# Optimization experiments

Measured on AMD Instinct MI355X. Metric: run time of the kernel, lower is better.

The kernel has to match this reference:

```python
import jax, jax.numpy as jnp
import numpy as np

BLANK = 0
NEG = jnp.float32(-1e30)  # finite stand-in for -inf (keeps logaddexp grads NaN-free)


def _ctc_loss(preds, targets, blank=BLANK):
    """CTC loss with fused log_softmax, zero_infinity, reduction='mean'.

    preds:   (N, T, C) raw logits
    targets: (N, L) int labels, 0 = padding/blank; target_lengths = count_nonzero
    """
    N, T, C = preds.shape
    L = targets.shape[1]
    S = 2 * L + 1  # extended label length (blanks interleaved)

    lp = jax.nn.log_softmax(preds, axis=-1)  # (N, T, C)

    # extended label sequence: blank, y1, blank, y2, ..., yL, blank
    ext = jnp.full((N, S), blank, dtype=targets.dtype).at[:, 1::2].set(targets)

    # gather log-probs of extended labels: (N, T, S) -> scan over T as (T, N, S)
    lp_ext = jax.vmap(lambda l, e: l[:, e])(lp, ext).transpose(1, 0, 2)

    # skip transition s-2 -> s allowed iff ext[s] != blank and ext[s] != ext[s-2]
    prev2 = jnp.pad(ext, ((0, 0), (2, 0)), constant_values=blank)[:, :S]
    skip_ok = (ext != blank) & (ext != prev2)  # (N, S)

    # alpha init at t=0
    alpha0 = jnp.full((N, S), NEG, dtype=lp.dtype)
    alpha0 = alpha0.at[:, 0].set(lp_ext[0, :, 0]).at[:, 1].set(lp_ext[0, :, 1])

    neg_col = jnp.full((N, 1), NEG, dtype=lp.dtype)

    def step(alpha, lp_t):
        a1 = jnp.concatenate([neg_col, alpha[:, :-1]], axis=1)
        a2 = jnp.concatenate([neg_col, neg_col, alpha[:, :-2]], axis=1)
        a2 = jnp.where(skip_ok, a2, NEG)
        alpha = jnp.logaddexp(jnp.logaddexp(alpha, a1), a2) + lp_t
        return alpha, None

    alpha, _ = jax.lax.scan(step, alpha0, lp_ext[1:])  # (N, S) at t = T-1

    tl = jnp.sum(targets != 0, axis=1)  # target lengths (pred lengths are all T)
    rows = jnp.arange(N)
    final = jnp.logaddexp(alpha[rows, 2 * tl], alpha[rows, 2 * tl - 1])

    # zero_infinity=True: zero out non-finite (vanished) losses
    loss = jnp.where(final < -1e29, 0.0, -final)
    # reduction='mean': divide each by its target length, then batch-mean
    return jnp.mean(loss / jnp.maximum(tl, 1).astype(loss.dtype))


def setup_inputs() -> dict:
    key = jax.random.key(0)
    k1, k2 = jax.random.split(key)
    preds = jax.random.normal(k1, (128, 1024, 256), dtype=jnp.float32)
    # labels in [1, C): nonzero so count_nonzero gives full target lengths
    targets = jax.random.randint(k2, (128, 128), 1, 256, dtype=jnp.int32)
    return {"preds": preds, "targets": targets}


def reference(preds, targets):
    return _ctc_loss(preds, targets)
```

## Files before the change

### kernel.cpp

```cpp
#include <hip/hip_runtime.h>

#define L2E 1.4426950408889634f
#define LN2D 0.6931471805599453

__device__ __forceinline__ void async_copy16(const float* g, float* l) {
    __builtin_amdgcn_global_load_lds(
        (const __attribute__((address_space(1))) void*)g,
        (__attribute__((address_space(3))) void*)l, 16, 0, 0);
}
__device__ __forceinline__ void wait_vm14() { __builtin_amdgcn_s_waitcnt(0x0F7E); }

__device__ __forceinline__ double dpp_sr1_f64(double x) {
    const int lo = __builtin_amdgcn_update_dpp(0, __double2loint(x), 0x138, 0xF, 0xF, true);
    const int hi = __builtin_amdgcn_update_dpp(0, __double2hiint(x), 0x138, 0xF, 0xF, true);
    return __hiloint2double(hi, lo);
}

__device__ __forceinline__ int wave_imax(int v) {
    int t;
#define DM(ctrl) t = __builtin_amdgcn_update_dpp(v, v, (ctrl), 0xF, 0xF, false); v = (v > t) ? v : t
    DM(0x111); DM(0x112); DM(0x114); DM(0x118);
    DM(0x142); DM(0x143);
#undef DM
    return __builtin_amdgcn_readlane(v, 63);
}

__global__ __launch_bounds__(256) void gather_kernel(const float* __restrict__ preds,
                                                     const int* __restrict__ targets,
                                                     float* __restrict__ gath,
                                                     float* __restrict__ blank) {
    constexpr int T = 1024, C = 256, L = 128;
    const int n = blockIdx.x >> 6;
    const int c = ((blockIdx.x & 63) << 2) + (threadIdx.x >> 6);
    const int lane = threadIdx.x & 63;
    const int w = threadIdx.x >> 6;

    const float* __restrict__ P = preds + ((size_t)n * T + (size_t)c * 4) * C;
    const int* __restrict__ tg = targets + (size_t)n * L;
    const int tgA = tg[2 * lane + 0];
    const int tgB = tg[2 * lane + 1];

    __shared__ float sRow[4][4][C];
    float m_k[4], r_k[4];
#pragma unroll
    for (int k = 0; k < 4; ++k) {
        const float4 v = reinterpret_cast<const float4*>(P + (size_t)k * C)[lane];
        reinterpret_cast<float4*>(&sRow[w][k][0])[lane] = v;
        float m = fmaxf(fmaxf(v.x, v.y), fmaxf(v.z, v.w));
#pragma unroll
        for (int off = 32; off; off >>= 1) m = fmaxf(m, __shfl_xor(m, off, 64));
        float s = exp2f((v.x - m) * L2E) + exp2f((v.y - m) * L2E) +
                  exp2f((v.z - m) * L2E) + exp2f((v.w - m) * L2E);
#pragma unroll
        for (int off = 32; off; off >>= 1) s += __shfl_xor(s, off, 64);
        m_k[k] = m; r_k[k] = 1.0f / s;
    }
    float4 gA, gB;
    gA.x = exp2f((sRow[w][0][tgA] - m_k[0]) * L2E) * r_k[0];
    gA.y = exp2f((sRow[w][1][tgA] - m_k[1]) * L2E) * r_k[1];
    gA.z = exp2f((sRow[w][2][tgA] - m_k[2]) * L2E) * r_k[2];
    gA.w = exp2f((sRow[w][3][tgA] - m_k[3]) * L2E) * r_k[3];
    gB.x = exp2f((sRow[w][0][tgB] - m_k[0]) * L2E) * r_k[0];
    gB.y = exp2f((sRow[w][1][tgB] - m_k[1]) * L2E) * r_k[1];
    gB.z = exp2f((sRow[w][2][tgB] - m_k[2]) * L2E) * r_k[2];
    gB.w = exp2f((sRow[w][3][tgB] - m_k[3]) * L2E) * r_k[3];

    float* gp = gath + ((size_t)n * 256 + c) * 512;
    *reinterpret_cast<float4*>(gp + 4 * lane) = gA;
    *reinterpret_cast<float4*>(gp + 256 + 4 * lane) = gB;
    if (lane == 0) {
        float4 b;
        b.x = exp2f((sRow[w][0][0] - m_k[0]) * L2E) * r_k[0];
        b.y = exp2f((sRow[w][1][0] - m_k[1]) * L2E) * r_k[1];
        b.z = exp2f((sRow[w][2][0] - m_k[2]) * L2E) * r_k[2];
        b.w = exp2f((sRow[w][3][0] - m_k[3]) * L2E) * r_k[3];
        *reinterpret_cast<float4*>(blank + (size_t)n * T + (size_t)c * 4) = b;
    }
}

__global__ __launch_bounds__(64) void ctc_alpha_kernel(const float* __restrict__ gath,
                                                       const float* __restrict__ blank,
                                                       const int* __restrict__ targets,
                                                       float* __restrict__ loss_out) {
    constexpr int T = 1024, L = 128, DIST = 8;
    __shared__ float sG[16 * 512];
    __shared__ float sBlank[T];
    __shared__ double sFin[257];

    const int n = blockIdx.x;
    const int lane = threadIdx.x;
    const int* __restrict__ tg = targets + (size_t)n * L;

    const int tA = tg[2 * lane + 0];
    const int tB = tg[2 * lane + 1];
    int tPrev = __shfl_up(tB, 1, 64);
    if (lane == 0) tPrev = 0;
    const bool skipA = (tA != 0) && (tA != tPrev);
    const bool skipB = (tB != 0) && (tB != tA);

    int cnt = (tA != 0) + (tB != 0);
#pragma unroll
    for (int off = 32; off; off >>= 1) cnt += __shfl_xor(cnt, off, 64);
    const int tl = cnt;

    const float* __restrict__ gn = gath + (size_t)n * 131072;
    const float* __restrict__ bn = blank + (size_t)n * T;

#pragma unroll
    for (int i = 0; i < 4; ++i) async_copy16(bn + i * 256 + lane * 4, &sBlank[i * 256]);
#pragma unroll
    for (int c = 0; c < DIST; ++c) {
        async_copy16(gn + c * 512 + lane * 4, &sG[c * 512]);
        async_copy16(gn + c * 512 + 256 + lane * 4, &sG[c * 512 + 256]);
    }

    double A0, A1, A2, A3, A4;
    double sc = 1.0;
    int e_apply = 0, K = 0;

#define LOADCHUNK(CC, AF, BF, BB) do {                                          \
        wait_vm14();                                                            \
        const int slot_ = (CC) & 15;                                            \
        AF = *reinterpret_cast<const float4*>(&sG[slot_ * 512 + 4 * lane]);     \
        BF = *reinterpret_cast<const float4*>(&sG[slot_ * 512 + 256 + 4 * lane]); \
        BB = *reinterpret_cast<const float4*>(&sBlank[4 * (CC)]);               \
        const int cp_ = (CC) + DIST, sp_ = cp_ & 15;                            \
        async_copy16(gn + cp_ * 512 + lane * 4, &sG[sp_ * 512]);                \
        async_copy16(gn + cp_ * 512 + 256 + lane * 4, &sG[sp_ * 512 + 256]);    \
    } while (0)

#define STEP(PB, PA, PB2) do {                                                  \
        const double p3 = dpp_sr1_f64(A3);                                      \
        const double u0 = A0 + p3;                                              \
        const double u1 = A1 + A0 + (skipA ? p3 : 0.0);                         \
        const double u2 = A2 + A1;                                              \
        const double u3 = A3 + A2 + (skipB ? A1 : 0.0);                         \
        const double u4 = A4 + A3;                                              \
        A0 = u0 * (PB); A1 = u1 * (PA); A2 = u2 * (PB);                         \
        A3 = u3 * (PB2); A4 = u4 * (PB);                                        \
    } while (0)

#define DOCHUNK(CC) do {                                                        \
        float4 Af_, Bf_, bb_;                                                   \
        LOADCHUNK(CC, Af_, Bf_, bb_);                                           \
        STEP((double)bb_.x, (double)Af_.x, (double)Bf_.x);                      \
        STEP((double)bb_.y, (double)Af_.y, (double)Bf_.y);                      \
        STEP((double)bb_.z, (double)Af_.z, (double)Bf_.z);                      \
        STEP((double)bb_.w, (double)Af_.w, (double)Bf_.w);                      \
    } while (0)

#define RESCALE() do {                                                          \
        A0 *= sc; A1 *= sc; A2 *= sc; A3 *= sc; A4 *= sc; K += e_apply;         \
        const double m_ = fmax(fmax(fmax(A0, A1), fmax(A2, A3)), A4);           \
        int e_ = ((__double2hiint(m_) >> 20) & 0x7FF) - 1023;                   \
        e_ = wave_imax(e_);                                                     \
        e_ = e_ < -960 ? -960 : (e_ > 960 ? 960 : e_);                          \
        e_apply = e_;                                                           \
        sc = __hiloint2double((1023 - e_) << 20, 0);                            \
    } while (0)

    {
        float4 Af_, Bf_, bb_;
        LOADCHUNK(0, Af_, Bf_, bb_);
        A0 = lane ? 0.0 : (double)bb_.x;
        A1 = lane ? 0.0 : (double)Af_.x;
        A2 = 0.0; A3 = 0.0; A4 = 0.0;
        STEP((double)bb_.y, (double)Af_.y, (double)Bf_.y);
        STEP((double)bb_.z, (double)Af_.z, (double)Bf_.z);
        STEP((double)bb_.w, (double)Af_.w, (double)Bf_.w);
    }
    for (int c = 1; c < 255; c += 2) {
        DOCHUNK(c);
        RESCALE();
        DOCHUNK(c + 1);
    }
    DOCHUNK(255);
    RESCALE();
#undef RESCALE
#undef DOCHUNK
#undef STEP
#undef LOADCHUNK

    sFin[4 * lane + 0] = A0; sFin[4 * lane + 1] = A1;
    sFin[4 * lane + 2] = A2; sFin[4 * lane + 3] = A3;
    if (lane == 63) sFin[256] = A4;
    __syncthreads();
    if (lane == 0) {
        int i1 = 2 * tl;
        int i0 = 2 * tl - 1;
        if (i0 < 0) i0 += 257;
        if (i1 > 256) i1 = 256;
        const double fin = sFin[i1] + sFin[i0];
        const double loss = (fin > 0.0) ? -(log2(fin) + (double)K) * LN2D : 0.0;
        loss_out[n] = (float)(loss / (double)(tl > 0 ? tl : 1));
    }
}

__global__ __launch_bounds__(64) void reduce_kernel(const float* __restrict__ loss,
                                                    float* __restrict__ out, int N) {
    float s = 0.0f;
    for (int i = threadIdx.x; i < N; i += 64) s += loss[i];
#pragma unroll
    for (int off = 32; off; off >>= 1) s += __shfl_xor(s, off, 64);
    if (threadIdx.x == 0) out[0] = s / (float)N;
}

extern "C" void kernel_launch(void* const* d_in, const int* in_sizes, int n_in,
                              void* d_out, int out_size, void* d_ws, size_t ws_size,
                              hipStream_t stream) {
    const float* preds = (const float*)d_in[0];
    const int* targets = (const int*)d_in[1];
    const int N = in_sizes[1] / 128;
    const int T = 1024;

    float* gath = (float*)d_ws;
    float* blank = gath + (size_t)N * 131072;
    float* loss = blank + (size_t)N * T;
    float* out = (float*)d_out;

    gather_kernel<<<N * 64, 256, 0, stream>>>(preds, targets, gath, blank);
    ctc_alpha_kernel<<<N, 64, 0, stream>>>(gath, blank, targets, loss);
    reduce_kernel<<<1, 64, 0, stream>>>(loss, out, N);
}
```

Baseline: 282.2 us.

## Split CTC recursion into interleaved forward-alpha and backward-beta halves

The single forward alpha recursion over all 1024 timesteps becomes a forward alpha pass over the first half and a backward beta pass over the second half. The two independent chains are interleaved step by step, and the loss is formed from a wave-reduced dot product of alpha and beta at the midpoint. This halves the serial dependency chain and exposes instruction-level parallelism. The cost is double register state and separate rescaling for each chain. Async prefetch now streams chunks from both ends of the gathered buffer.

```diff
diff --git a/kernel.cpp b/kernel.cpp
--- a/kernel.cpp
+++ b/kernel.cpp
@@ -8,14 +8,19 @@
         (const __attribute__((address_space(1))) void*)g,
         (__attribute__((address_space(3))) void*)l, 16, 0, 0);
 }
-__device__ __forceinline__ void wait_vm14() { __builtin_amdgcn_s_waitcnt(0x0F7E); }
+__device__ __forceinline__ void wait_vm28() { __builtin_amdgcn_s_waitcnt(0x4F7C); }
+__device__ __forceinline__ void wait_vm0()  { __builtin_amdgcn_s_waitcnt(0x0F70); }
 
 __device__ __forceinline__ double dpp_sr1_f64(double x) {
     const int lo = __builtin_amdgcn_update_dpp(0, __double2loint(x), 0x138, 0xF, 0xF, true);
     const int hi = __builtin_amdgcn_update_dpp(0, __double2hiint(x), 0x138, 0xF, 0xF, true);
     return __hiloint2double(hi, lo);
 }
-
+__device__ __forceinline__ double dpp_sl1_f64(double x) {
+    const int lo = __builtin_amdgcn_update_dpp(0, __double2loint(x), 0x130, 0xF, 0xF, true);
+    const int hi = __builtin_amdgcn_update_dpp(0, __double2hiint(x), 0x130, 0xF, 0xF, true);
+    return __hiloint2double(hi, lo);
+}
 __device__ __forceinline__ int wave_imax(int v) {
     int t;
 #define DM(ctrl) t = __builtin_amdgcn_update_dpp(v, v, (ctrl), 0xF, 0xF, false); v = (v > t) ? v : t
@@ -82,10 +87,9 @@
                                                        const float* __restrict__ blank,
                                                        const int* __restrict__ targets,
                                                        float* __restrict__ loss_out) {
-    constexpr int T = 1024, L = 128, DIST = 8;
+    constexpr int T = 1024, L = 128;
     __shared__ float sG[16 * 512];
     __shared__ float sBlank[T];
-    __shared__ double sFin[257];
 
     const int n = blockIdx.x;
     const int lane = threadIdx.x;
@@ -95,41 +99,50 @@
     const int tB = tg[2 * lane + 1];
     int tPrev = __shfl_up(tB, 1, 64);
     if (lane == 0) tPrev = 0;
-    const bool skipA = (tA != 0) && (tA != tPrev);
+    const int skipAi = (tA != 0 && tA != tPrev) ? 1 : 0;
+    const bool skipA = skipAi != 0;
     const bool skipB = (tB != 0) && (tB != tA);
+    const double mBd = skipB ? 1.0 : 0.0;
+    const double mA1d = (double)__shfl_down(skipAi, 1, 64);
 
     int cnt = (tA != 0) + (tB != 0);
 #pragma unroll
     for (int off = 32; off; off >>= 1) cnt += __shfl_xor(cnt, off, 64);
     const int tl = cnt;
+    int i1 = 2 * tl;       if (i1 > 256) i1 = 256;
+    int i0 = 2 * tl - 1;   if (i0 < 0) i0 += 257;
 
     const float* __restrict__ gn = gath + (size_t)n * 131072;
     const float* __restrict__ bn = blank + (size_t)n * T;
 
+    wait_vm0();
+
 #pragma unroll
     for (int i = 0; i < 4; ++i) async_copy16(bn + i * 256 + lane * 4, &sBlank[i * 256]);
 #pragma unroll
-    for (int c = 0; c < DIST; ++c) {
-        async_copy16(gn + c * 512 + lane * 4, &sG[c * 512]);
-        async_copy16(gn + c * 512 + 256 + lane * 4, &sG[c * 512 + 256]);
+    for (int i = 0; i < 8; ++i) {
+        async_copy16(gn + i * 512 + lane * 4,       &sG[i * 512]);
+        async_copy16(gn + i * 512 + 256 + lane * 4, &sG[i * 512 + 256]);
+        const int q = 255 - i;
+        async_copy16(gn + q * 512 + lane * 4,       &sG[(8 + i) * 512]);
+        async_copy16(gn + q * 512 + 256 + lane * 4, &sG[(8 + i) * 512 + 256]);
     }
 
     double A0, A1, A2, A3, A4;
-    double sc = 1.0;
-    int e_apply = 0, K = 0;
-
-#define LOADCHUNK(CC, AF, BF, BB) do {                                          \
-        wait_vm14();                                                            \
-        const int slot_ = (CC) & 15;                                            \
-        AF = *reinterpret_cast<const float4*>(&sG[slot_ * 512 + 4 * lane]);     \
-        BF = *reinterpret_cast<const float4*>(&sG[slot_ * 512 + 256 + 4 * lane]); \
-        BB = *reinterpret_cast<const float4*>(&sBlank[4 * (CC)]);               \
-        const int cp_ = (CC) + DIST, sp_ = cp_ & 15;                            \
-        async_copy16(gn + cp_ * 512 + lane * 4, &sG[sp_ * 512]);                \
-        async_copy16(gn + cp_ * 512 + 256 + lane * 4, &sG[sp_ * 512 + 256]);    \
-    } while (0)
-
-#define STEP(PB, PA, PB2) do {                                                  \
+    double B0, B1, B2, B3, B4;
+    double scA = 1.0, scB = 1.0;
+    int eA = 0, eB = 0, KA = 0, KB = 0;
+
+    {
+        const int s0 = 4 * lane;
+        B0 = (s0 == i1 || s0 == i0) ? 1.0 : 0.0;
+        B1 = (s0 + 1 == i1 || s0 + 1 == i0) ? 1.0 : 0.0;
+        B2 = (s0 + 2 == i1 || s0 + 2 == i0) ? 1.0 : 0.0;
+        B3 = (s0 + 3 == i1 || s0 + 3 == i0) ? 1.0 : 0.0;
+        B4 = (lane == 63 && (i1 == 256 || i0 == 256)) ? 1.0 : 0.0;
+    }
+
+#define ASTEP(PB, PA, PB2) do {                                                 \
         const double p3 = dpp_sr1_f64(A3);                                      \
         const double u0 = A0 + p3;                                              \
         const double u1 = A1 + A0 + (skipA ? p3 : 0.0);                         \
@@ -140,58 +153,88 @@
         A3 = u3 * (PB2); A4 = u4 * (PB);                                        \
     } while (0)
 
-#define DOCHUNK(CC) do {                                                        \
-        float4 Af_, Bf_, bb_;                                                   \
-        LOADCHUNK(CC, Af_, Bf_, bb_);                                           \
-        STEP((double)bb_.x, (double)Af_.x, (double)Bf_.x);                      \
-        STEP((double)bb_.y, (double)Af_.y, (double)Bf_.y);                      \
-        STEP((double)bb_.z, (double)Af_.z, (double)Bf_.z);                      \
-        STEP((double)bb_.w, (double)Af_.w, (double)Bf_.w);                      \
-    } while (0)
-
-#define RESCALE() do {                                                          \
-        A0 *= sc; A1 *= sc; A2 *= sc; A3 *= sc; A4 *= sc; K += e_apply;         \
-        const double m_ = fmax(fmax(fmax(A0, A1), fmax(A2, A3)), A4);           \
-        int e_ = ((__double2hiint(m_) >> 20) & 0x7FF) - 1023;                   \
-        e_ = wave_imax(e_);                                                     \
-        e_ = e_ < -960 ? -960 : (e_ > 960 ? 960 : e_);                          \
-        e_apply = e_;                                                           \
-        sc = __hiloint2double((1023 - e_) << 20, 0);                            \
-    } while (0)
-
-    {
-        float4 Af_, Bf_, bb_;
-        LOADCHUNK(0, Af_, Bf_, bb_);
-        A0 = lane ? 0.0 : (double)bb_.x;
-        A1 = lane ? 0.0 : (double)Af_.x;
-        A2 = 0.0; A3 = 0.0; A4 = 0.0;
-        STEP((double)bb_.y, (double)Af_.y, (double)Bf_.y);
-        STEP((double)bb_.z, (double)Af_.z, (double)Bf_.z);
-        STEP((double)bb_.w, (double)Af_.w, (double)Bf_.w);
-    }
-    for (int c = 1; c < 255; c += 2) {
-        DOCHUNK(c);
-        RESCALE();
-        DOCHUNK(c + 1);
-    }
-    DOCHUNK(255);
-    RESCALE();
-#undef RESCALE
-#undef DOCHUNK
-#undef STEP
-#undef LOADCHUNK
-
-    sFin[4 * lane + 0] = A0; sFin[4 * lane + 1] = A1;
-    sFin[4 * lane + 2] = A2; sFin[4 * lane + 3] = A3;
-    if (lane == 63) sFin[256] = A4;
-    __syncthreads();
+#define BSTEP(PBF, PAF, PBF2) do {                                              \
+        const double pb_ = (PBF);                                               \
+        const double g0 = pb_ * B0;                                             \
+        const double g1 = (PAF) * B1;                                           \
+        const double g2 = pb_ * B2;                                             \
+        const double g3 = (PBF2) * B3;                                          \
+        const double g4 = pb_ * B4;                                             \
+        double G4 = dpp_sl1_f64(g0);                                            \
+        G4 = (lane == 63) ? g4 : G4;                                            \
+        const double G5 = dpp_sl1_f64(g1);                                      \
+        B0 = g0 + g1;                                                           \
+        B1 = fma(mBd, g3, g1 + g2);                                             \
+        B2 = g2 + g3;                                                           \
+        B3 = fma(mA1d, G5, g3 + G4);                                            \
+        B4 = g4;                                                                \
+    } while (0)
+
+#define PAIRBODY(P_, FIRST_)  do {                                              \
+        const int sl_ = (P_) & 7;                                               \
+        wait_vm28();                                                            \
+        const float4 aA = *reinterpret_cast<const float4*>(&sG[sl_ * 512 + 4 * lane]);        \
+        const float4 aB = *reinterpret_cast<const float4*>(&sG[sl_ * 512 + 256 + 4 * lane]);  \
+        const float4 ab = *reinterpret_cast<const float4*>(&sBlank[4 * (P_)]);                \
+        const float4 bA = *reinterpret_cast<const float4*>(&sG[(8 + sl_) * 512 + 4 * lane]);       \
+        const float4 bB = *reinterpret_cast<const float4*>(&sG[(8 + sl_) * 512 + 256 + 4 * lane]); \
+        const float4 bb = *reinterpret_cast<const float4*>(&sBlank[4 * (255 - (P_))]);        \
+        { const int cp = (P_) + 8, q = 247 - (P_);                              \
+          async_copy16(gn + cp * 512 + lane * 4,       &sG[sl_ * 512]);         \
+          async_copy16(gn + cp * 512 + 256 + lane * 4, &sG[sl_ * 512 + 256]);   \
+          async_copy16(gn + q * 512 + lane * 4,        &sG[(8 + sl_) * 512]);   \
+          async_copy16(gn + q * 512 + 256 + lane * 4,  &sG[(8 + sl_) * 512 + 256]); } \
+        if (FIRST_) {                                                           \
+            A0 = lane ? 0.0 : (double)ab.x;                                     \
+            A1 = lane ? 0.0 : (double)aA.x;                                     \
+            A2 = 0.0; A3 = 0.0; A4 = 0.0;                                       \
+        } else {                                                                \
+            ASTEP((double)ab.x, (double)aA.x, (double)aB.x);                    \
+        }                                                                       \
+        BSTEP((double)bb.w, (double)bA.w, (double)bB.w);                        \
+        ASTEP((double)ab.y, (double)aA.y, (double)aB.y);                        \
+        BSTEP((double)bb.z, (double)bA.z, (double)bB.z);                        \
+        ASTEP((double)ab.z, (double)aA.z, (double)aB.z);                        \
+        BSTEP((double)bb.y, (double)bA.y, (double)bB.y);                        \
+        ASTEP((double)ab.w, (double)aA.w, (double)aB.w);                        \
+        BSTEP((double)bb.x, (double)bA.x, (double)bB.x);                        \
+    } while (0)
+
+#define RESCALES() do {                                                         \
+        A0 *= scA; A1 *= scA; A2 *= scA; A3 *= scA; A4 *= scA; KA += eA;        \
+        B0 *= scB; B1 *= scB; B2 *= scB; B3 *= scB; B4 *= scB; KB += eB;        \
+        const double ma = fmax(fmax(fmax(A0, A1), fmax(A2, A3)), A4);           \
+        const double mb = fmax(fmax(fmax(B0, B1), fmax(B2, B3)), B4);           \
+        int ea_ = ((__double2hiint(ma) >> 20) & 0x7FF) - 1023;                  \
+        int eb_ = ((__double2hiint(mb) >> 20) & 0x7FF) - 1023;                  \
+        ea_ = wave_imax(ea_); eb_ = wave_imax(eb_);                             \
+        ea_ = ea_ < -960 ? -960 : (ea_ > 960 ? 960 : ea_);                      \
+        eb_ = eb_ < -960 ? -960 : (eb_ > 960 ? 960 : eb_);                      \
+        eA = ea_; scA = __hiloint2double((1023 - ea_) << 20, 0);                \
+        eB = eb_; scB = __hiloint2double((1023 - eb_) << 20, 0);                \
+    } while (0)
+
+    PAIRBODY(0, true);
+    for (int p = 1; p < 127; p += 2) {
+        PAIRBODY(p, false);
+        RESCALES();
+        PAIRBODY(p + 1, false);
+    }
+    PAIRBODY(127, false);
+    RESCALES();
+    A0 *= scA; A1 *= scA; A2 *= scA; A3 *= scA; A4 *= scA; KA += eA;
+    B0 *= scB; B1 *= scB; B2 *= scB; B3 *= scB; B4 *= scB; KB += eB;
+#undef RESCALES
+#undef PAIRBODY
+#undef BSTEP
+#undef ASTEP
+
+    double S = A0 * B0 + A1 * B1 + A2 * B2 + A3 * B3;
+    S += (lane == 63) ? A4 * B4 : 0.0;
+#pragma unroll
+    for (int off = 32; off; off >>= 1) S += __shfl_xor(S, off, 64);
     if (lane == 0) {
-        int i1 = 2 * tl;
-        int i0 = 2 * tl - 1;
-        if (i0 < 0) i0 += 257;
-        if (i1 > 256) i1 = 256;
-        const double fin = sFin[i1] + sFin[i0];
-        const double loss = (fin > 0.0) ? -(log2(fin) + (double)K) * LN2D : 0.0;
+        const double loss = (S > 0.0) ? -(log2(S) + (double)(KA + KB)) * LN2D : 0.0;
         loss_out[n] = (float)(loss / (double)(tl > 0 ? tl : 1));
     }
 }
```

Result: faster. 265.5 us (-5.9%).

## Fuse softmax-gather into CTC recursion with split forward/backward halves and producer waves

Applied to the files above, without the earlier changes.

Replaces the separate gather kernel and alpha kernel with one fused kernel. Three producer waves compute the softmax and gathered probabilities for 4-timestep chunks into shared-memory slots, while one consumer wave runs the recursion. Each utterance is split across two blocks: one runs the forward alpha pass over the first half of time and the other runs a backward beta pass from the final states over the second half. A combine kernel then takes the dot product of the two halves to get each loss. This removes the large gathered intermediate from global memory and halves the serial dependency chain per block. In exchange it adds per-round block barriers and a more intricate final combine.

```diff
diff --git a/kernel.cpp b/kernel.cpp
--- a/kernel.cpp
+++ b/kernel.cpp
@@ -8,14 +8,19 @@
         (const __attribute__((address_space(1))) void*)g,
         (__attribute__((address_space(3))) void*)l, 16, 0, 0);
 }
-__device__ __forceinline__ void wait_vm14() { __builtin_amdgcn_s_waitcnt(0x0F7E); }
+__device__ __forceinline__ void wait_vm0() { __builtin_amdgcn_s_waitcnt(0x0F70); }
+__device__ __forceinline__ void wait_vm4() { __builtin_amdgcn_s_waitcnt(0x0F74); }
 
 __device__ __forceinline__ double dpp_sr1_f64(double x) {
     const int lo = __builtin_amdgcn_update_dpp(0, __double2loint(x), 0x138, 0xF, 0xF, true);
     const int hi = __builtin_amdgcn_update_dpp(0, __double2hiint(x), 0x138, 0xF, 0xF, true);
     return __hiloint2double(hi, lo);
 }
-
+__device__ __forceinline__ double dpp_sl1_f64(double x) {
+    const int lo = __builtin_amdgcn_update_dpp(0, __double2loint(x), 0x130, 0xF, 0xF, true);
+    const int hi = __builtin_amdgcn_update_dpp(0, __double2hiint(x), 0x130, 0xF, 0xF, true);
+    return __hiloint2double(hi, lo);
+}
 __device__ __forceinline__ int wave_imax(int v) {
     int t;
 #define DM(ctrl) t = __builtin_amdgcn_update_dpp(v, v, (ctrl), 0xF, 0xF, false); v = (v > t) ? v : t
@@ -25,27 +30,13 @@
     return __builtin_amdgcn_readlane(v, 63);
 }
 
-__global__ __launch_bounds__(256) void gather_kernel(const float* __restrict__ preds,
-                                                     const int* __restrict__ targets,
-                                                     float* __restrict__ gath,
-                                                     float* __restrict__ blank) {
-    constexpr int T = 1024, C = 256, L = 128;
-    const int n = blockIdx.x >> 6;
-    const int c = ((blockIdx.x & 63) << 2) + (threadIdx.x >> 6);
-    const int lane = threadIdx.x & 63;
-    const int w = threadIdx.x >> 6;
-
-    const float* __restrict__ P = preds + ((size_t)n * T + (size_t)c * 4) * C;
-    const int* __restrict__ tg = targets + (size_t)n * L;
-    const int tgA = tg[2 * lane + 0];
-    const int tgB = tg[2 * lane + 1];
-
-    __shared__ float sRow[4][4][C];
-    float m_k[4], r_k[4];
+__device__ __forceinline__ void produce_chunk(const float* __restrict__ row,
+                                              float* __restrict__ slot,
+                                              int lane, int tA, int tB) {
+    float mk[4], rk[4];
 #pragma unroll
     for (int k = 0; k < 4; ++k) {
-        const float4 v = reinterpret_cast<const float4*>(P + (size_t)k * C)[lane];
-        reinterpret_cast<float4*>(&sRow[w][k][0])[lane] = v;
+        const float4 v = *reinterpret_cast<const float4*>(&row[k * 256 + 4 * lane]);
         float m = fmaxf(fmaxf(v.x, v.y), fmaxf(v.z, v.w));
 #pragma unroll
         for (int off = 32; off; off >>= 1) m = fmaxf(m, __shfl_xor(m, off, 64));
@@ -53,156 +44,231 @@
                   exp2f((v.z - m) * L2E) + exp2f((v.w - m) * L2E);
 #pragma unroll
         for (int off = 32; off; off >>= 1) s += __shfl_xor(s, off, 64);
-        m_k[k] = m; r_k[k] = 1.0f / s;
+        mk[k] = m; rk[k] = 1.0f / s;
     }
     float4 gA, gB;
-    gA.x = exp2f((sRow[w][0][tgA] - m_k[0]) * L2E) * r_k[0];
-    gA.y = exp2f((sRow[w][1][tgA] - m_k[1]) * L2E) * r_k[1];
-    gA.z = exp2f((sRow[w][2][tgA] - m_k[2]) * L2E) * r_k[2];
-    gA.w = exp2f((sRow[w][3][tgA] - m_k[3]) * L2E) * r_k[3];
-    gB.x = exp2f((sRow[w][0][tgB] - m_k[0]) * L2E) * r_k[0];
-    gB.y = exp2f((sRow[w][1][tgB] - m_k[1]) * L2E) * r_k[1];
-    gB.z = exp2f((sRow[w][2][tgB] - m_k[2]) * L2E) * r_k[2];
-    gB.w = exp2f((sRow[w][3][tgB] - m_k[3]) * L2E) * r_k[3];
-
-    float* gp = gath + ((size_t)n * 256 + c) * 512;
-    *reinterpret_cast<float4*>(gp + 4 * lane) = gA;
-    *reinterpret_cast<float4*>(gp + 256 + 4 * lane) = gB;
+    gA.x = exp2f((row[0 * 256 + tA] - mk[0]) * L2E) * rk[0];
+    gA.y = exp2f((row[1 * 256 + tA] - mk[1]) * L2E) * rk[1];
+    gA.z = exp2f((row[2 * 256 + tA] - mk[2]) * L2E) * rk[2];
+    gA.w = exp2f((row[3 * 256 + tA] - mk[3]) * L2E) * rk[3];
+    gB.x = exp2f((row[0 * 256 + tB] - mk[0]) * L2E) * rk[0];
+    gB.y = exp2f((row[1 * 256 + tB] - mk[1]) * L2E) * rk[1];
+    gB.z = exp2f((row[2 * 256 + tB] - mk[2]) * L2E) * rk[2];
+    gB.w = exp2f((row[3 * 256 + tB] - mk[3]) * L2E) * rk[3];
+    *reinterpret_cast<float4*>(&slot[4 * lane]) = gA;
+    *reinterpret_cast<float4*>(&slot[256 + 4 * lane]) = gB;
     if (lane == 0) {
-        float4 b;
-        b.x = exp2f((sRow[w][0][0] - m_k[0]) * L2E) * r_k[0];
-        b.y = exp2f((sRow[w][1][0] - m_k[1]) * L2E) * r_k[1];
-        b.z = exp2f((sRow[w][2][0] - m_k[2]) * L2E) * r_k[2];
-        b.w = exp2f((sRow[w][3][0] - m_k[3]) * L2E) * r_k[3];
-        *reinterpret_cast<float4*>(blank + (size_t)n * T + (size_t)c * 4) = b;
-    }
-}
-
-__global__ __launch_bounds__(64) void ctc_alpha_kernel(const float* __restrict__ gath,
-                                                       const float* __restrict__ blank,
-                                                       const int* __restrict__ targets,
-                                                       float* __restrict__ loss_out) {
-    constexpr int T = 1024, L = 128, DIST = 8;
-    __shared__ float sG[16 * 512];
-    __shared__ float sBlank[T];
-    __shared__ double sFin[257];
-
-    const int n = blockIdx.x;
-    const int lane = threadIdx.x;
+        float4 bb;
+        bb.x = exp2f((row[0 * 256] - mk[0]) * L2E) * rk[0];
+        bb.y = exp2f((row[1 * 256] - mk[1]) * L2E) * rk[1];
+        bb.z = exp2f((row[2 * 256] - mk[2]) * L2E) * rk[2];
+        bb.w = exp2f((row[3 * 256] - mk[3]) * L2E) * rk[3];
+        *reinterpret_cast<float4*>(&slot[512]) = bb;
+    }
+}
+
+__global__ __launch_bounds__(256) void ctc_fused_kernel(
+        const float* __restrict__ preds, const int* __restrict__ targets,
+        double* __restrict__ Aws, double* __restrict__ Bws, int* __restrict__ meta) {
+    constexpr int T = 1024, L = 128, NCH = 128;
+    __shared__ float sSlot[6][520];
+    __shared__ float sRowBuf[3][2][4 * 256];
+
+    const int n = blockIdx.x >> 1;
+    const int h = blockIdx.x & 1;
+    const int wv = threadIdx.x >> 6;
+    const int lane = threadIdx.x & 63;
+
     const int* __restrict__ tg = targets + (size_t)n * L;
-
     const int tA = tg[2 * lane + 0];
     const int tB = tg[2 * lane + 1];
+    const float* __restrict__ Pn = preds + (size_t)n * T * 256;
+
     int tPrev = __shfl_up(tB, 1, 64);
     if (lane == 0) tPrev = 0;
-    const bool skipA = (tA != 0) && (tA != tPrev);
+    const int skipAi = (tA != 0 && tA != tPrev) ? 1 : 0;
+    const bool skipA = skipAi != 0;
     const bool skipB = (tB != 0) && (tB != tA);
-
+    const double mBd = skipB ? 1.0 : 0.0;
+    const double mA1d = (double)__shfl_down(skipAi, 1, 64);
     int cnt = (tA != 0) + (tB != 0);
 #pragma unroll
     for (int off = 32; off; off >>= 1) cnt += __shfl_xor(cnt, off, 64);
     const int tl = cnt;
-
-    const float* __restrict__ gn = gath + (size_t)n * 131072;
-    const float* __restrict__ bn = blank + (size_t)n * T;
-
-#pragma unroll
-    for (int i = 0; i < 4; ++i) async_copy16(bn + i * 256 + lane * 4, &sBlank[i * 256]);
-#pragma unroll
-    for (int c = 0; c < DIST; ++c) {
-        async_copy16(gn + c * 512 + lane * 4, &sG[c * 512]);
-        async_copy16(gn + c * 512 + 256 + lane * 4, &sG[c * 512 + 256]);
-    }
-
-    double A0, A1, A2, A3, A4;
+    int i1 = 2 * tl;     if (i1 > 256) i1 = 256;
+    int i0 = 2 * tl - 1; if (i0 < 0) i0 += 257;
+
+    double X0 = 0.0, X1 = 0.0, X2 = 0.0, X3 = 0.0, X4 = 0.0;
+    if (h == 1) {
+        const int s0 = 4 * lane;
+        X0 = (s0 == i1 || s0 == i0) ? 1.0 : 0.0;
+        X1 = (s0 + 1 == i1 || s0 + 1 == i0) ? 1.0 : 0.0;
+        X2 = (s0 + 2 == i1 || s0 + 2 == i0) ? 1.0 : 0.0;
+        X3 = (s0 + 3 == i1 || s0 + 3 == i0) ? 1.0 : 0.0;
+        X4 = (lane == 63 && (i1 == 256 || i0 == 256)) ? 1.0 : 0.0;
+    }
     double sc = 1.0;
     int e_apply = 0, K = 0;
 
-#define LOADCHUNK(CC, AF, BF, BB) do {                                          \
-        wait_vm14();                                                            \
-        const int slot_ = (CC) & 15;                                            \
-        AF = *reinterpret_cast<const float4*>(&sG[slot_ * 512 + 4 * lane]);     \
-        BF = *reinterpret_cast<const float4*>(&sG[slot_ * 512 + 256 + 4 * lane]); \
-        BB = *reinterpret_cast<const float4*>(&sBlank[4 * (CC)]);               \
-        const int cp_ = (CC) + DIST, sp_ = cp_ & 15;                            \
-        async_copy16(gn + cp_ * 512 + lane * 4, &sG[sp_ * 512]);                \
-        async_copy16(gn + cp_ * 512 + 256 + lane * 4, &sG[sp_ * 512 + 256]);    \
+#define ASTEP(PBf, PAf, PB2f) do {                                              \
+        const double PB = (double)(PBf), PA = (double)(PAf), PB2 = (double)(PB2f); \
+        const double p3 = dpp_sr1_f64(X3);                                      \
+        const double u0 = X0 + p3;                                              \
+        const double u1 = X1 + X0 + (skipA ? p3 : 0.0);                         \
+        const double u2 = X2 + X1;                                              \
+        const double u3 = X3 + X2 + (skipB ? X1 : 0.0);                         \
+        const double u4 = X4 + X3;                                              \
+        X0 = u0 * PB; X1 = u1 * PA; X2 = u2 * PB; X3 = u3 * PB2; X4 = u4 * PB;  \
     } while (0)
 
-#define STEP(PB, PA, PB2) do {                                                  \
-        const double p3 = dpp_sr1_f64(A3);                                      \
-        const double u0 = A0 + p3;                                              \
-        const double u1 = A1 + A0 + (skipA ? p3 : 0.0);                         \
-        const double u2 = A2 + A1;                                              \
-        const double u3 = A3 + A2 + (skipB ? A1 : 0.0);                         \
-        const double u4 = A4 + A3;                                              \
-        A0 = u0 * (PB); A1 = u1 * (PA); A2 = u2 * (PB);                         \
-        A3 = u3 * (PB2); A4 = u4 * (PB);                                        \
+#define BSTEP(PBf, PAf, PB2f) do {                                              \
+        const double pb_ = (double)(PBf);                                       \
+        const double g0 = pb_ * X0;                                             \
+        const double g1 = (double)(PAf) * X1;                                   \
+        const double g2 = pb_ * X2;                                             \
+        const double g3 = (double)(PB2f) * X3;                                  \
+        const double g4 = pb_ * X4;                                             \
+        double G4 = dpp_sl1_f64(g0);                                            \
+        G4 = (lane == 63) ? g4 : G4;                                            \
+        const double G5 = dpp_sl1_f64(g1);                                      \
+        X0 = g0 + g1;                                                           \
+        X1 = fma(mBd, g3, g1 + g2);                                             \
+        X2 = g2 + g3;                                                           \
+        X3 = fma(mA1d, G5, g3 + G4);                                            \
+        X4 = g4;                                                                \
     } while (0)
 
-#define DOCHUNK(CC) do {                                                        \
-        float4 Af_, Bf_, bb_;                                                   \
-        LOADCHUNK(CC, Af_, Bf_, bb_);                                           \
-        STEP((double)bb_.x, (double)Af_.x, (double)Bf_.x);                      \
-        STEP((double)bb_.y, (double)Af_.y, (double)Bf_.y);                      \
-        STEP((double)bb_.z, (double)Af_.z, (double)Bf_.z);                      \
-        STEP((double)bb_.w, (double)Af_.w, (double)Bf_.w);                      \
-    } while (0)
-
 #define RESCALE() do {                                                          \
-        A0 *= sc; A1 *= sc; A2 *= sc; A3 *= sc; A4 *= sc; K += e_apply;         \
-        const double m_ = fmax(fmax(fmax(A0, A1), fmax(A2, A3)), A4);           \
+        X0 *= sc; X1 *= sc; X2 *= sc; X3 *= sc; X4 *= sc; K += e_apply;         \
+        const double m_ = fmax(fmax(fmax(X0, X1), fmax(X2, X3)), X4);           \
         int e_ = ((__double2hiint(m_) >> 20) & 0x7FF) - 1023;                   \
         e_ = wave_imax(e_);                                                     \
         e_ = e_ < -960 ? -960 : (e_ > 960 ? 960 : e_);                          \
-        e_apply = e_;                                                           \
-        sc = __hiloint2double((1023 - e_) << 20, 0);                            \
+        e_apply = e_; sc = __hiloint2double((1023 - e_) << 20, 0);              \
     } while (0)
 
-    {
-        float4 Af_, Bf_, bb_;
-        LOADCHUNK(0, Af_, Bf_, bb_);
-        A0 = lane ? 0.0 : (double)bb_.x;
-        A1 = lane ? 0.0 : (double)Af_.x;
-        A2 = 0.0; A3 = 0.0; A4 = 0.0;
-        STEP((double)bb_.y, (double)Af_.y, (double)Bf_.y);
-        STEP((double)bb_.z, (double)Af_.z, (double)Bf_.z);
-        STEP((double)bb_.w, (double)Af_.w, (double)Bf_.w);
-    }
-    for (int c = 1; c < 255; c += 2) {
-        DOCHUNK(c);
-        RESCALE();
-        DOCHUNK(c + 1);
-    }
-    DOCHUNK(255);
-    RESCALE();
+    wait_vm0();
+
+    if (wv > 0) {
+        const int pw = wv - 1;
+        const int gc0 = h ? 255 - pw : pw;
+#pragma unroll
+        for (int k = 0; k < 4; ++k)
+            async_copy16(Pn + (size_t)(4 * gc0 + k) * 256 + 4 * lane, &sRowBuf[pw][0][k * 256]);
+        wait_vm0();
+        produce_chunk(&sRowBuf[pw][0][0], &sSlot[pw][0], lane, tA, tB);
+        const int gc1 = h ? 255 - (pw + 3) : (pw + 3);
+#pragma unroll
+        for (int k = 0; k < 4; ++k)
+            async_copy16(Pn + (size_t)(4 * gc1 + k) * 256 + 4 * lane, &sRowBuf[pw][1][k * 256]);
+    }
+    __syncthreads();
+
+    for (int r = 0; r < 43; ++r) {
+        if (wv > 0) {
+            const int pw = wv - 1;
+            const int cp = 3 * (r + 1) + pw;
+            const int cn = cp + 3;
+            if (cn < NCH) {
+                const int gcn = h ? 255 - cn : cn;
+                float* dst = &sRowBuf[pw][r & 1][0];
+#pragma unroll
+                for (int k = 0; k < 4; ++k)
+                    async_copy16(Pn + (size_t)(4 * gcn + k) * 256 + 4 * lane, dst + k * 256);
+            }
+            if (cp < NCH) {
+                if (cn < NCH) wait_vm4(); else wait_vm0();
+                const int slot = pw + (((r + 1) & 1) ? 3 : 0);
+                produce_chunk(&sRowBuf[pw][(r + 1) & 1][0], &sSlot[slot][0], lane, tA, tB);
+            }
+        } else {
+            const int sb = (r & 1) ? 3 : 0;
+            {
+                const float4 fA = *reinterpret_cast<const float4*>(&sSlot[sb][4 * lane]);
+                const float4 fB = *reinterpret_cast<const float4*>(&sSlot[sb][256 + 4 * lane]);
+                const float4 fb = *reinterpret_cast<const float4*>(&sSlot[sb][512]);
+                if (h == 0) {
+                    if (r == 0) {
+                        X0 = lane ? 0.0 : (double)fb.x;
+                        X1 = lane ? 0.0 : (double)fA.x;
+                        X2 = 0.0; X3 = 0.0; X4 = 0.0;
+                    } else ASTEP(fb.x, fA.x, fB.x);
+                    ASTEP(fb.y, fA.y, fB.y); ASTEP(fb.z, fA.z, fB.z); ASTEP(fb.w, fA.w, fB.w);
+                } else {
+                    BSTEP(fb.w, fA.w, fB.w); BSTEP(fb.z, fA.z, fB.z);
+                    BSTEP(fb.y, fA.y, fB.y); BSTEP(fb.x, fA.x, fB.x);
+                }
+            }
+            {
+                const float4 fA = *reinterpret_cast<const float4*>(&sSlot[sb + 1][4 * lane]);
+                const float4 fB = *reinterpret_cast<const float4*>(&sSlot[sb + 1][256 + 4 * lane]);
+                const float4 fb = *reinterpret_cast<const float4*>(&sSlot[sb + 1][512]);
+                if (h == 0) {
+                    ASTEP(fb.x, fA.x, fB.x); ASTEP(fb.y, fA.y, fB.y);
+                    ASTEP(fb.z, fA.z, fB.z); ASTEP(fb.w, fA.w, fB.w);
+                } else {
+                    BSTEP(fb.w, fA.w, fB.w); BSTEP(fb.z, fA.z, fB.z);
+                    BSTEP(fb.y, fA.y, fB.y); BSTEP(fb.x, fA.x, fB.x);
+                }
+            }
+            if (3 * r + 2 < NCH) {
+                const float4 fA = *reinterpret_cast<const float4*>(&sSlot[sb + 2][4 * lane]);
+                const float4 fB = *reinterpret_cast<const float4*>(&sSlot[sb + 2][256 + 4 * lane]);
+                const float4 fb = *reinterpret_cast<const float4*>(&sSlot[sb + 2][512]);
+                if (h == 0) {
+                    ASTEP(fb.x, fA.x, fB.x); ASTEP(fb.y, fA.y, fB.y);
+                    ASTEP(fb.z, fA.z, fB.z); ASTEP(fb.w, fA.w, fB.w);
+                } else {
+                    BSTEP(fb.w, fA.w, fB.w); BSTEP(fb.z, fA.z, fB.z);
+                    BSTEP(fb.y, fA.y, fB.y); BSTEP(fb.x, fA.x, fB.x);
+                }
+            }
+            RESCALE();
+        }
+        __syncthreads();
+    }
 #undef RESCALE
-#undef DOCHUNK
-#undef STEP
-#undef LOADCHUNK
-
-    sFin[4 * lane + 0] = A0; sFin[4 * lane + 1] = A1;
-    sFin[4 * lane + 2] = A2; sFin[4 * lane + 3] = A3;
-    if (lane == 63) sFin[256] = A4;
+#undef BSTEP
+#undef ASTEP
+
+    if (wv == 0) {
+        X0 *= sc; X1 *= sc; X2 *= sc; X3 *= sc; X4 *= sc; K += e_apply;
+        double* __restrict__ W = (h ? Bws : Aws) + (size_t)n * 260;
+        double4 st; st.x = X0; st.y = X1; st.z = X2; st.w = X3;
+        *reinterpret_cast<double4*>(&W[4 * lane]) = st;
+        if (lane == 63) W[256] = X4;
+        if (lane == 0) {
+            if (h == 0) { meta[4 * n + 0] = K; meta[4 * n + 2] = tl; }
+            else          meta[4 * n + 1] = K;
+        }
+    }
+}
+
+__global__ __launch_bounds__(256) void combine_kernel(const double* __restrict__ Aws,
+                                                      const double* __restrict__ Bws,
+                                                      const int* __restrict__ meta,
+                                                      float* __restrict__ out, int N) {
+    __shared__ double sPart[4];
+    const int wv = threadIdx.x >> 6, lane = threadIdx.x & 63;
+    double acc = 0.0;
+    for (int n = wv; n < N; n += 4) {
+        const double* A = Aws + (size_t)n * 260;
+        const double* B = Bws + (size_t)n * 260;
+        const double4 a = *reinterpret_cast<const double4*>(&A[4 * lane]);
+        const double4 b = *reinterpret_cast<const double4*>(&B[4 * lane]);
+        double S = a.x * b.x + a.y * b.y + a.z * b.z + a.w * b.w;
+        if (lane == 63) S += A[256] * B[256];
+#pragma unroll
+        for (int off = 32; off; off >>= 1) S += __shfl_xor(S, off, 64);
+        const int Ksum = meta[4 * n] + meta[4 * n + 1];
+        const int tl = meta[4 * n + 2];
+        const double loss = (S > 0.0) ? -(log2(S) + (double)Ksum) * LN2D : 0.0;
+        acc += loss / (double)(tl > 0 ? tl : 1);
+    }
+    if (lane == 0) sPart[wv] = acc;
     __syncthreads();
-    if (lane == 0) {
-        int i1 = 2 * tl;
-        int i0 = 2 * tl - 1;
-        if (i0 < 0) i0 += 257;
-        if (i1 > 256) i1 = 256;
-        const double fin = sFin[i1] + sFin[i0];
-        const double loss = (fin > 0.0) ? -(log2(fin) + (double)K) * LN2D : 0.0;
-        loss_out[n] = (float)(loss / (double)(tl > 0 ? tl : 1));
-    }
-}
-
-__global__ __launch_bounds__(64) void reduce_kernel(const float* __restrict__ loss,
-                                                    float* __restrict__ out, int N) {
-    float s = 0.0f;
-    for (int i = threadIdx.x; i < N; i += 64) s += loss[i];
-#pragma unroll
-    for (int off = 32; off; off >>= 1) s += __shfl_xor(s, off, 64);
-    if (threadIdx.x == 0) out[0] = s / (float)N;
+    if (threadIdx.x == 0)
+        out[0] = (float)((sPart[0] + sPart[1] + sPart[2] + sPart[3]) / (double)N);
 }
 
 extern "C" void kernel_launch(void* const* d_in, const int* in_sizes, int n_in,
@@ -211,14 +277,12 @@
     const float* preds = (const float*)d_in[0];
     const int* targets = (const int*)d_in[1];
     const int N = in_sizes[1] / 128;
-    const int T = 1024;
-
-    float* gath = (float*)d_ws;
-    float* blank = gath + (size_t)N * 131072;
-    float* loss = blank + (size_t)N * T;
+
+    double* Aws = (double*)d_ws;
+    double* Bws = Aws + (size_t)N * 260;
+    int* meta = (int*)(Bws + (size_t)N * 260);
     float* out = (float*)d_out;
 
-    gather_kernel<<<N * 64, 256, 0, stream>>>(preds, targets, gath, blank);
-    ctc_alpha_kernel<<<N, 64, 0, stream>>>(gath, blank, targets, loss);
-    reduce_kernel<<<1, 64, 0, stream>>>(loss, out, N);
-}
+    ctc_fused_kernel<<<2 * N, 256, 0, stream>>>(preds, targets, Aws, Bws, meta);
+    combine_kernel<<<1, 256, 0, stream>>>(Aws, Bws, meta, out, N);
+}
```

Result: no change. 283.7 us (+0.5%).
